# Kernel optimization log

Measured on AMD Instinct MI355X. Metric: run time of the kernel, lower is better.

Reference implementation:

```python
import jax, jax.numpy as jnp
import numpy as np

B, S, DM, DH, H, R = 2, 4096, 512, 512, 8, 4
HD = DH // H
SCALING = 1.0 / R  # alpha / r = 1.0 / 4


def setup_inputs() -> dict:
    key = jax.random.key(0)
    ks = jax.random.split(key, 12)
    lim = 1.0 / np.sqrt(DM)  # kaiming_uniform(a=sqrt(5)) bound for fan_in=DM
    inp = {
        "x": jax.random.normal(ks[0], (B, S, DM), dtype=jnp.float32),
        "atten_mask": jax.random.randint(ks[1], (B, S), 0, 2, dtype=jnp.int32),
        "Wk": jax.random.uniform(ks[2], (DH, DM), jnp.float32, -lim, lim),
        "Wq": jax.random.uniform(ks[3], (DH, DM), jnp.float32, -lim, lim),
        "Wv": jax.random.uniform(ks[4], (DH, DM), jnp.float32, -lim, lim),
        "Aq": jax.random.normal(ks[5], (R, DM), dtype=jnp.float32) * 0.01,
        "Bq": jax.random.normal(ks[6], (DH, R), dtype=jnp.float32) * 0.01,
        "Av": jax.random.normal(ks[7], (R, DM), dtype=jnp.float32) * 0.01,
        "Bv": jax.random.normal(ks[8], (DH, R), dtype=jnp.float32) * 0.01,
        "Wp": jax.random.uniform(ks[9], (DM, DH), jnp.float32, -1.0 / np.sqrt(DH), 1.0 / np.sqrt(DH)),
        "bp": jax.random.uniform(ks[10], (DM,), jnp.float32, -1.0 / np.sqrt(DH), 1.0 / np.sqrt(DH)),
    }
    return inp


def _heads(t):
    # [B,S,DH] -> [B,H,S,HD]
    return t.reshape(B, S, H, HD).transpose(0, 2, 1, 3)


def reference(x, atten_mask, Wk, Wq, Wv, Aq, Bq, Av, Bv, Wp, bp):
    k = x @ Wk.T
    q = x @ Wq.T + SCALING * ((x @ Aq.T) @ Bq.T)
    v = x @ Wv.T + SCALING * ((x @ Av.T) @ Bv.T)
    qh, kh, vh = _heads(q), _heads(k), _heads(v)
    scores = jnp.einsum("bhqd,bhkd->bhqk", qh, kh) / jnp.sqrt(jnp.float32(HD))
    neg = jnp.finfo(scores.dtype).min  # acts like -inf fill
    mask = (atten_mask == 0)[:, None, None, :]  # [B,1,1,S] over keys
    scores = jnp.where(mask, -jnp.inf, scores)
    probs = jax.nn.softmax(scores, axis=-1)
    ctx = jnp.einsum("bhqk,bhkd->bhqd", probs, vh)
    ctx = ctx.transpose(0, 2, 1, 3).reshape(B, S, DH)
    return ctx @ Wp.T + bp
```

## Files before the change

### kernel.cpp

```cpp
#include <hip/hip_runtime.h>
#include <hip/hip_bf16.h>
#include <stdint.h>

#define B_   2
#define S_   4096
#define DM_  512
#define DH_  512
#define H_   8
#define BS_  (B_*S_)
#define NX_  (BS_*DM_)
#define NW_  (DM_*DH_)
#define LOG2E 1.4426950408889634f
#define QSCALE (0.125f*LOG2E)

typedef __attribute__((ext_vector_type(4))) float f32x4;
typedef __attribute__((ext_vector_type(4))) short s16x4;
typedef __attribute__((ext_vector_type(8))) short s16x8;

__device__ __forceinline__ short f2bf(float x){
  uint32_t u = __builtin_bit_cast(uint32_t, x);
  u = (u + 0x7fffu + ((u >> 16) & 1u)) >> 16;
  return (short)u;
}
__device__ __forceinline__ float exp2fast(float x){ return __builtin_amdgcn_exp2f(x); }

__global__ __launch_bounds__(256) void convlora_kernel(
    const float* __restrict__ x,  const float* __restrict__ Wk,
    const float* __restrict__ Wq, const float* __restrict__ Wv,
    const float* __restrict__ Wp, const int* __restrict__ mask,
    const float* __restrict__ Aq, const float* __restrict__ Av,
    short* __restrict__ xbf,  short* __restrict__ wkbf, short* __restrict__ wqbf,
    short* __restrict__ wvbf, short* __restrict__ wpbf,
    float* __restrict__ biasw, float* __restrict__ Uq, float* __restrict__ Uv)
{
  const int bid = blockIdx.x;
  if (bid < 2560){
    const int tid = bid*256 + threadIdx.x;
    if (tid < BS_) biasw[tid] = mask[tid] ? 0.f : -1e30f;
    size_t idx = (size_t)tid*8;
    const float* src; short* dst; size_t off;
    if (idx < NX_)                      { src=x;  dst=xbf;  off=idx; }
    else if (idx < NX_+(size_t)NW_)     { src=Wk; dst=wkbf; off=idx-NX_; }
    else if (idx < NX_+2*(size_t)NW_)   { src=Wq; dst=wqbf; off=idx-NX_-NW_; }
    else if (idx < NX_+3*(size_t)NW_)   { src=Wv; dst=wvbf; off=idx-NX_-2*(size_t)NW_; }
    else                                { src=Wp; dst=wpbf; off=idx-NX_-3*(size_t)NW_; }
    f32x4 a = *(const f32x4*)(src+off);
    f32x4 b = *(const f32x4*)(src+off+4);
    s16x8 o;
    o[0]=f2bf(a.x); o[1]=f2bf(a.y); o[2]=f2bf(a.z); o[3]=f2bf(a.w);
    o[4]=f2bf(b.x); o[5]=f2bf(b.y); o[6]=f2bf(b.z); o[7]=f2bf(b.w);
    *(s16x8*)(dst+off) = o;
  } else {
    const int lane = threadIdx.x & 63, w = threadIdx.x >> 6;
    const int row = (bid-2560)*4 + w;
    const f32x4* xp = (const f32x4*)(x + (size_t)row*DM_ + lane*8);
    f32x4 x0 = xp[0], x1 = xp[1];
    float acc[8];
    #pragma unroll
    for (int r=0;r<4;r++){
      const f32x4* ap = (const f32x4*)(Aq + r*DM_ + lane*8);
      f32x4 a0 = ap[0], a1 = ap[1];
      const f32x4* vp = (const f32x4*)(Av + r*DM_ + lane*8);
      f32x4 b0 = vp[0], b1 = vp[1];
      acc[r]   = x0.x*a0.x + x0.y*a0.y + x0.z*a0.z + x0.w*a0.w
               + x1.x*a1.x + x1.y*a1.y + x1.z*a1.z + x1.w*a1.w;
      acc[4+r] = x0.x*b0.x + x0.y*b0.y + x0.z*b0.z + x0.w*b0.w
               + x1.x*b1.x + x1.y*b1.y + x1.z*b1.z + x1.w*b1.w;
    }
    #pragma unroll
    for (int i=0;i<8;i++){
      float v = acc[i];
      #pragma unroll
      for (int m=1;m<64;m<<=1) v += __shfl_xor(v, m);
      acc[i] = v;
    }
    if (lane == 0){
      #pragma unroll
      for (int r=0;r<4;r++){ Uq[row*4+r] = acc[r]; Uv[row*4+r] = acc[4+r]; }
    }
  }
}

__global__ __launch_bounds__(256) void qkv_kernel(
    const short* __restrict__ xbf,
    const short* __restrict__ wkbf, const short* __restrict__ wqbf,
    const short* __restrict__ wvbf,
    const float* __restrict__ Uq, const float* __restrict__ Bq,
    const float* __restrict__ Uv, const float* __restrict__ Bv,
    short* __restrict__ kw, short* __restrict__ qw, short* __restrict__ vw)
{
  __shared__ __align__(16) short As[128*32];
  __shared__ __align__(16) short Bsm[64*32];
  const int t = threadIdx.x;
  const int lane = t & 63, w = t >> 6;
  const int g = lane >> 4, l15 = lane & 15;
  const int m0 = blockIdx.x * 128;
  const int proj = blockIdx.y >> 3;
  const int n0 = (blockIdx.y & 7) * 64;
  const short* W = proj==0 ? wkbf : (proj==1 ? wqbf : wvbf);

  f32x4 acc[2][4];
  #pragma unroll
  for (int i=0;i<2;i++)
    #pragma unroll
    for (int j=0;j<4;j++){ f32x4 z = {0.f,0.f,0.f,0.f}; acc[i][j] = z; }

  const int rA0 = t >> 2,        sA0 = t & 3;
  const int rA1 = (t+256) >> 2,  sA1 = t & 3;
  const int rB  = t >> 2,        sB  = t & 3;

  const short* pa0 = xbf + (size_t)(m0+rA0)*DM_ + sA0*8;
  const short* pa1 = xbf + (size_t)(m0+rA1)*DM_ + sA1*8;
  const short* pbp = W   + (size_t)(n0+rB )*DM_ + sB *8;
  short* wa0 = (short*)((char*)As  + rA0*64 + ((sA0 ^ (rA0&3))*16));
  short* wa1 = (short*)((char*)As  + rA1*64 + ((sA1 ^ (rA1&3))*16));
  short* wb  = (short*)((char*)Bsm + rB *64 + ((sB  ^ (rB &3))*16));

  s16x8 va0 = *(const s16x8*)pa0; pa0 += 32;
  s16x8 va1 = *(const s16x8*)pa1; pa1 += 32;
  s16x8 vb  = *(const s16x8*)pbp; pbp += 32;

  for (int kt=0; kt<16; ++kt){
    __syncthreads();
    *(s16x8*)wa0 = va0;
    *(s16x8*)wa1 = va1;
    *(s16x8*)wb  = vb;
    __syncthreads();

    if (kt+1 < 16){
      va0 = *(const s16x8*)pa0; pa0 += 32;
      va1 = *(const s16x8*)pa1; pa1 += 32;
      vb  = *(const s16x8*)pbp; pbp += 32;
    }

    s16x8 af[2], bfr[4];
    #pragma unroll
    for (int mf=0; mf<2; ++mf){
      int rr = w*32 + mf*16 + l15;
      af[mf] = *(const s16x8*)((const char*)As + rr*64 + ((g ^ (rr&3))*16));
    }
    #pragma unroll
    for (int nf=0; nf<4; ++nf){
      int rr = nf*16 + l15;
      bfr[nf] = *(const s16x8*)((const char*)Bsm + rr*64 + ((g ^ (rr&3))*16));
    }
    __builtin_amdgcn_s_setprio(1);
    #pragma unroll
    for (int mf=0; mf<2; ++mf)
      #pragma unroll
      for (int nf=0; nf<4; ++nf)
        acc[mf][nf] = __builtin_amdgcn_mfma_f32_16x16x32_bf16(af[mf], bfr[nf], acc[mf][nf], 0, 0, 0);
    __builtin_amdgcn_s_setprio(0);
  }

  short* outp = proj==0 ? kw : (proj==1 ? qw : vw);
  const float* Um = (proj==1) ? Uq : Uv;
  const float* Bm = (proj==1) ? Bq : Bv;
  #pragma unroll
  for (int mf=0; mf<2; ++mf){
    #pragma unroll
    for (int r=0; r<4; ++r){
      const int m = m0 + w*32 + mf*16 + g*4 + r;
      f32x4 uvec = {0.f,0.f,0.f,0.f};
      if (proj) uvec = *(const f32x4*)(Um + m*4);
      #pragma unroll
      for (int nf=0; nf<4; ++nf){
        const int cn = n0 + nf*16 + l15;
        float val = acc[mf][nf][r];
        if (proj){
          f32x4 bb = *(const f32x4*)(Bm + cn*4);
          val += 0.25f*(uvec.x*bb.x + uvec.y*bb.y + uvec.z*bb.z + uvec.w*bb.w);
        }
        if (proj==1) val *= QSCALE;
        outp[(size_t)m*DH_ + cn] = f2bf(val);
      }
    }
  }
}

__global__ __launch_bounds__(256) void vt_kernel(const short* __restrict__ vw, short* __restrict__ vt){
  __shared__ __align__(16) short T[64*72];
  const int t = threadIdx.x;
  const int st = blockIdx.x, bh = blockIdx.y;
  const int b = bh >> 3, h = bh & 7;
  #pragma unroll
  for (int p=0;p<2;p++){
    int c = t + p*256;
    int row = c >> 3, off = c & 7;
    s16x8 v = *(const s16x8*)(vw + (size_t)(b*S_ + st*64 + row)*DH_ + h*64 + off*8);
    *(s16x8*)((char*)T + row*144 + off*16) = v;
  }
  __syncthreads();
  #pragma unroll
  for (int p=0;p<2;p++){
    int c = t + p*256;
    int d = c >> 3, soff = c & 7;
    s16x8 o;
    #pragma unroll
    for (int j=0;j<8;j++)
      o[j] = *((const short*)((const char*)T + (soff*8+j)*144 + d*2));
    *(s16x8*)(vt + (size_t)(bh*64 + d)*S_ + st*64 + soff*8) = o;
  }
}

__global__ __launch_bounds__(256) void attn_kernel(
    const short* __restrict__ qw, const short* __restrict__ kw,
    const short* __restrict__ vtw, const float* __restrict__ biasw,
    short* __restrict__ ctxw)
{
  __shared__ __align__(16) char smem[32768];
  short* Ks = (short*)smem;
  short* Vs = (short*)(smem + 8192);
  char*  Ps = smem + 16384;
  const int t = threadIdx.x, lane = t & 63, w = t >> 6;
  const int g = lane >> 4, l15 = lane & 15;
  const int bid = blockIdx.x;
  const int xcd = bid & 7, jj = bid >> 3;
  const int bh = xcd*2 + (jj >> 5), qb = jj & 31;
  const int b = bh >> 3, h = bh & 7;
  const int qr0 = qb*128 + w*32;

  s16x8 qf[2][2];
  #pragma unroll
  for (int tile=0;tile<2;tile++)
    #pragma unroll
    for (int ks=0;ks<2;ks++)
      qf[tile][ks] = *(const s16x8*)(qw + (size_t)(b*S_ + qr0 + tile*16 + l15)*DH_
                                     + h*64 + ks*32 + g*8);

  const float* gb = biasw + b*S_ + g*4;
  const short* kbase = kw + (size_t)(b*S_)*DH_ + h*64;
  const short* vbase = vtw + (size_t)(bh*64)*S_;
  char* Pw = Ps + w*4096;

  f32x4 ctx[2][5];
  #pragma unroll
  for (int tile=0;tile<2;tile++)
    #pragma unroll
    for (int n=0;n<5;n++){ f32x4 z = {0.f,0.f,0.f,0.f}; ctx[tile][n] = z; }

  const s16x8 ones = { 0x3F80,0x3F80,0x3F80,0x3F80,0x3F80,0x3F80,0x3F80,0x3F80 };

  const int c1 = t + 256;
  const int r0 = t >> 3,  o0 = t & 7;
  const int r1 = c1 >> 3, o1 = c1 & 7;
  const short* kp0 = kbase + (size_t)r0*DH_ + o0*8;
  const short* kp1 = kbase + (size_t)r1*DH_ + o1*8;
  const short* vp0 = vbase + (size_t)r0*S_ + o0*8;
  const short* vp1 = vbase + (size_t)r1*S_ + o1*8;
  char* wk0 = (char*)Ks + r0*128 + ((o0 ^ (r0&7))*16);
  char* wk1 = (char*)Ks + r1*128 + ((o1 ^ (r1&7))*16);
  char* wv0 = (char*)Vs + r0*128 + ((o0 ^ (r0&7))*16);
  char* wv1 = (char*)Vs + r1*128 + ((o1 ^ (r1&7))*16);

  s16x8 kv0 = *(const s16x8*)kp0; kp0 += 64*DH_;
  s16x8 kv1 = *(const s16x8*)kp1; kp1 += 64*DH_;
  s16x8 vv0 = *(const s16x8*)vp0; vp0 += 64;
  s16x8 vv1 = *(const s16x8*)vp1; vp1 += 64;
  f32x4 bvn[4];
  #pragma unroll
  for (int sb=0; sb<4; ++sb) bvn[sb] = *(const f32x4*)(gb + sb*16);

  for (int kt=0; kt<64; ++kt){
    __syncthreads();
    *(s16x8*)wk0 = kv0; *(s16x8*)wk1 = kv1;
    *(s16x8*)wv0 = vv0; *(s16x8*)wv1 = vv1;
    __syncthreads();

    f32x4 bv[4];
    #pragma unroll
    for (int sb=0; sb<4; ++sb) bv[sb] = bvn[sb];

    if (kt+1 < 64){
      kv0 = *(const s16x8*)kp0; kp0 += 64*DH_;
      kv1 = *(const s16x8*)kp1; kp1 += 64*DH_;
      vv0 = *(const s16x8*)vp0; vp0 += 64;
      vv1 = *(const s16x8*)vp1; vp1 += 64;
      const float* gn = gb + (kt+1)*64;
      #pragma unroll
      for (int sb=0; sb<4; ++sb) bvn[sb] = *(const f32x4*)(gn + sb*16);
    }

    f32x4 stA[4], stB[4];
    __builtin_amdgcn_s_setprio(1);
    #pragma unroll
    for (int sb=0; sb<4; ++sb){
      f32x4 sA = bv[sb], sB = bv[sb];
      #pragma unroll
      for (int ks=0; ks<2; ++ks){
        int row = sb*16 + l15;
        s16x8 kf = *(const s16x8*)((const char*)Ks + row*128 + (((ks*4+g) ^ (row&7))*16));
        sA = __builtin_amdgcn_mfma_f32_16x16x32_bf16(kf, qf[0][ks], sA, 0, 0, 0);
        sB = __builtin_amdgcn_mfma_f32_16x16x32_bf16(kf, qf[1][ks], sB, 0, 0, 0);
      }
      stA[sb] = sA; stB[sb] = sB;
    }
    __builtin_amdgcn_s_setprio(0);

    #pragma unroll
    for (int sb=0; sb<4; ++sb){
      int slot = (sb*2 + (g>>1)) ^ (l15 & 7);
      char* base = Pw + l15*128 + slot*16 + (g&1)*8;
      union { __hip_bfloat16 h[4]; s16x4 v; } cvA, cvB;
      cvA.h[0] = __float2bfloat16(exp2fast(stA[sb][0]));
      cvA.h[1] = __float2bfloat16(exp2fast(stA[sb][1]));
      cvA.h[2] = __float2bfloat16(exp2fast(stA[sb][2]));
      cvA.h[3] = __float2bfloat16(exp2fast(stA[sb][3]));
      cvB.h[0] = __float2bfloat16(exp2fast(stB[sb][0]));
      cvB.h[1] = __float2bfloat16(exp2fast(stB[sb][1]));
      cvB.h[2] = __float2bfloat16(exp2fast(stB[sb][2]));
      cvB.h[3] = __float2bfloat16(exp2fast(stB[sb][3]));
      *(s16x4*)(base)        = cvA.v;
      *(s16x4*)(base + 2048) = cvB.v;
    }

    __builtin_amdgcn_s_setprio(1);
    #pragma unroll
    for (int ks=0; ks<2; ++ks){
      const char* pb = Pw + l15*128 + (((ks*4+g) ^ (l15&7))*16);
      s16x8 pfA = *(const s16x8*)(pb);
      s16x8 pfB = *(const s16x8*)(pb + 2048);
      #pragma unroll
      for (int n=0;n<4;n++){
        int row = n*16 + l15;
        s16x8 vf = *(const s16x8*)((const char*)Vs + row*128 + (((ks*4+g) ^ (row&7))*16));
        ctx[0][n] = __builtin_amdgcn_mfma_f32_16x16x32_bf16(pfA, vf, ctx[0][n], 0, 0, 0);
        ctx[1][n] = __builtin_amdgcn_mfma_f32_16x16x32_bf16(pfB, vf, ctx[1][n], 0, 0, 0);
      }
      ctx[0][4] = __builtin_amdgcn_mfma_f32_16x16x32_bf16(pfA, ones, ctx[0][4], 0, 0, 0);
      ctx[1][4] = __builtin_amdgcn_mfma_f32_16x16x32_bf16(pfB, ones, ctx[1][4], 0, 0, 0);
    }
    __builtin_amdgcn_s_setprio(0);
  }

  #pragma unroll
  for (int tile=0;tile<2;tile++){
    float inv[4];
    #pragma unroll
    for (int r=0;r<4;r++) inv[r] = 1.f / ctx[tile][4][r];
    #pragma unroll
    for (int n=0;n<4;n++)
      #pragma unroll
      for (int r=0;r<4;r++){
        int m = b*S_ + qr0 + tile*16 + g*4 + r;
        ctxw[(size_t)m*DH_ + h*64 + n*16 + l15] = f2bf(ctx[tile][n][r] * inv[r]);
      }
  }
}

__global__ __launch_bounds__(256) void oproj_kernel(
    const short* __restrict__ ctxw, const short* __restrict__ wpbf,
    const float* __restrict__ bp, float* __restrict__ out)
{
  __shared__ __align__(16) short As[128*32];
  __shared__ __align__(16) short Bsm[64*32];
  const int t = threadIdx.x, lane = t & 63, w = t >> 6;
  const int g = lane >> 4, l15 = lane & 15;
  const int m0 = blockIdx.x*128, n0 = blockIdx.y*64;
  f32x4 acc[2][4];
  #pragma unroll
  for (int i=0;i<2;i++)
    #pragma unroll
    for (int j=0;j<4;j++){ f32x4 z = {0.f,0.f,0.f,0.f}; acc[i][j] = z; }

  const int rA0 = t >> 2,        sA0 = t & 3;
  const int rA1 = (t+256) >> 2,  sA1 = t & 3;
  const int rB  = t >> 2,        sB  = t & 3;

  const short* pa0 = ctxw + (size_t)(m0+rA0)*DH_ + sA0*8;
  const short* pa1 = ctxw + (size_t)(m0+rA1)*DH_ + sA1*8;
  const short* pbp = wpbf + (size_t)(n0+rB )*DH_ + sB *8;
  short* wa0 = (short*)((char*)As  + rA0*64 + ((sA0 ^ (rA0&3))*16));
  short* wa1 = (short*)((char*)As  + rA1*64 + ((sA1 ^ (rA1&3))*16));
  short* wb  = (short*)((char*)Bsm + rB *64 + ((sB  ^ (rB &3))*16));

  s16x8 va0 = *(const s16x8*)pa0; pa0 += 32;
  s16x8 va1 = *(const s16x8*)pa1; pa1 += 32;
  s16x8 vb  = *(const s16x8*)pbp; pbp += 32;

  for (int kt=0; kt<16; ++kt){
    __syncthreads();
    *(s16x8*)wa0 = va0;
    *(s16x8*)wa1 = va1;
    *(s16x8*)wb  = vb;
    __syncthreads();

    if (kt+1 < 16){
      va0 = *(const s16x8*)pa0; pa0 += 32;
      va1 = *(const s16x8*)pa1; pa1 += 32;
      vb  = *(const s16x8*)pbp; pbp += 32;
    }

    s16x8 af[2], bfr[4];
    #pragma unroll
    for (int mf=0; mf<2; ++mf){
      int rr = w*32 + mf*16 + l15;
      af[mf] = *(const s16x8*)((const char*)As + rr*64 + ((g ^ (rr&3))*16));
    }
    #pragma unroll
    for (int nf=0; nf<4; ++nf){
      int rr = nf*16 + l15;
      bfr[nf] = *(const s16x8*)((const char*)Bsm + rr*64 + ((g ^ (rr&3))*16));
    }
    __builtin_amdgcn_s_setprio(1);
    #pragma unroll
    for (int mf=0; mf<2; ++mf)
      #pragma unroll
      for (int nf=0; nf<4; ++nf)
        acc[mf][nf] = __builtin_amdgcn_mfma_f32_16x16x32_bf16(af[mf], bfr[nf], acc[mf][nf], 0, 0, 0);
    __builtin_amdgcn_s_setprio(0);
  }

  #pragma unroll
  for (int mf=0; mf<2; ++mf)
    #pragma unroll
    for (int nf=0; nf<4; ++nf){
      const int cn = n0 + nf*16 + l15;
      const float bpv = bp[cn];
      #pragma unroll
      for (int r=0;r<4;r++){
        const int m = m0 + w*32 + mf*16 + g*4 + r;
        out[(size_t)m*DM_ + cn] = acc[mf][nf][r] + bpv;
      }
    }
}

extern "C" void kernel_launch(void* const* d_in, const int* in_sizes, int n_in,
                              void* d_out, int out_size, void* d_ws, size_t ws_size,
                              hipStream_t stream)
{
  const float* x  = (const float*)d_in[0];
  const int* mask = (const int*)d_in[1];
  const float* Wk = (const float*)d_in[2];
  const float* Wq = (const float*)d_in[3];
  const float* Wv = (const float*)d_in[4];
  const float* Aq = (const float*)d_in[5];
  const float* Bq = (const float*)d_in[6];
  const float* Av = (const float*)d_in[7];
  const float* Bv = (const float*)d_in[8];
  const float* Wp = (const float*)d_in[9];
  const float* bp = (const float*)d_in[10];
  float* out = (float*)d_out;

  char* ws = (char*)d_ws;
  short* qw   = (short*)(ws);
  short* kw   = (short*)(ws + 8388608);
  short* vw   = (short*)(ws + 16777216);
  short* vtw  = (short*)(ws + 25165824);
  short* xbf  = (short*)(ws + 25165824);
  short* ctxw = (short*)(ws + 16777216);
  float* Uq   = (float*)(ws + 33554432);
  float* Uv   = (float*)(ws + 33685504);
  float* biasw= (float*)(ws + 33816576);
  short* wkbf = (short*)(ws + 33849344);
  short* wqbf = (short*)(ws + 34373632);
  short* wvbf = (short*)(ws + 34897920);
  short* wpbf = (short*)(ws + 35422208);

  convlora_kernel<<<dim3(4608), dim3(256), 0, stream>>>(
      x, Wk, Wq, Wv, Wp, mask, Aq, Av,
      xbf, wkbf, wqbf, wvbf, wpbf, biasw, Uq, Uv);
  qkv_kernel<<<dim3(64, 24), dim3(256), 0, stream>>>(xbf, wkbf, wqbf, wvbf,
                                                     Uq, Bq, Uv, Bv, kw, qw, vw);
  vt_kernel<<<dim3(64, 16), dim3(256), 0, stream>>>(vw, vtw);
  attn_kernel<<<dim3(512), dim3(256), 0, stream>>>(qw, kw, vtw, biasw, ctxw);
  oproj_kernel<<<dim3(64, 8), dim3(256), 0, stream>>>(ctxw, wpbf, bp, out);
  (void)in_sizes; (void)n_in; (void)out_size; (void)ws_size;
}
```

Measured before the change: 240.5 us.

## Split attention key range across two wave groups and merge partial results

```diff
diff --git a/kernel.cpp b/kernel.cpp
--- a/kernel.cpp
+++ b/kernel.cpp
@@ -203,22 +203,25 @@
   }
 }
 
-__global__ __launch_bounds__(256) void attn_kernel(
+__global__ __launch_bounds__(512) void attn_kernel(
     const short* __restrict__ qw, const short* __restrict__ kw,
     const short* __restrict__ vtw, const float* __restrict__ biasw,
     short* __restrict__ ctxw)
 {
-  __shared__ __align__(16) char smem[32768];
-  short* Ks = (short*)smem;
-  short* Vs = (short*)(smem + 8192);
-  char*  Ps = smem + 16384;
+  __shared__ __align__(16) char smem[65536];
   const int t = threadIdx.x, lane = t & 63, w = t >> 6;
   const int g = lane >> 4, l15 = lane & 15;
+  const int kvg = w >> 2, wq = w & 3;
   const int bid = blockIdx.x;
   const int xcd = bid & 7, jj = bid >> 3;
   const int bh = xcd*2 + (jj >> 5), qb = jj & 31;
   const int b = bh >> 3, h = bh & 7;
-  const int qr0 = qb*128 + w*32;
+  const int qr0 = qb*128 + wq*32;
+
+  short* Ks = (short*)(smem + kvg*16384);
+  short* Vs = (short*)(smem + kvg*16384 + 8192);
+  char*  Ps = smem + 32768;
+  char*  Pw = Ps + w*4096;
 
   s16x8 qf[2][2];
   #pragma unroll
@@ -228,10 +231,9 @@
       qf[tile][ks] = *(const s16x8*)(qw + (size_t)(b*S_ + qr0 + tile*16 + l15)*DH_
                                      + h*64 + ks*32 + g*8);
 
-  const float* gb = biasw + b*S_ + g*4;
-  const short* kbase = kw + (size_t)(b*S_)*DH_ + h*64;
-  const short* vbase = vtw + (size_t)(bh*64)*S_;
-  char* Pw = Ps + w*4096;
+  const float* gb = biasw + b*S_ + kvg*2048 + g*4;
+  const short* kbase = kw + (size_t)(b*S_ + kvg*2048)*DH_ + h*64;
+  const short* vbase = vtw + (size_t)(bh*64)*S_ + kvg*2048;
 
   f32x4 ctx[2][5];
   #pragma unroll
@@ -241,9 +243,10 @@
 
   const s16x8 ones = { 0x3F80,0x3F80,0x3F80,0x3F80,0x3F80,0x3F80,0x3F80,0x3F80 };
 
-  const int c1 = t + 256;
-  const int r0 = t >> 3,  o0 = t & 7;
-  const int r1 = c1 >> 3, o1 = c1 & 7;
+  const int tg = t & 255;
+  const int c1 = tg + 256;
+  const int r0 = tg >> 3,  o0 = tg & 7;
+  const int r1 = c1 >> 3,  o1 = c1 & 7;
   const short* kp0 = kbase + (size_t)r0*DH_ + o0*8;
   const short* kp1 = kbase + (size_t)r1*DH_ + o1*8;
   const short* vp0 = vbase + (size_t)r0*S_ + o0*8;
@@ -261,7 +264,7 @@
   #pragma unroll
   for (int sb=0; sb<4; ++sb) bvn[sb] = *(const f32x4*)(gb + sb*16);
 
-  for (int kt=0; kt<64; ++kt){
+  for (int kt=0; kt<32; ++kt){
     __syncthreads();
     *(s16x8*)wk0 = kv0; *(s16x8*)wk1 = kv1;
     *(s16x8*)wv0 = vv0; *(s16x8*)wv1 = vv1;
@@ -271,7 +274,7 @@
     #pragma unroll
     for (int sb=0; sb<4; ++sb) bv[sb] = bvn[sb];
 
-    if (kt+1 < 64){
+    if (kt+1 < 32){
       kv0 = *(const s16x8*)kp0; kp0 += 64*DH_;
       kv1 = *(const s16x8*)kp1; kp1 += 64*DH_;
       vv0 = *(const s16x8*)vp0; vp0 += 64;
@@ -333,18 +336,41 @@
     __builtin_amdgcn_s_setprio(0);
   }
 
-  #pragma unroll
-  for (int tile=0;tile<2;tile++){
-    float inv[4];
-    #pragma unroll
-    for (int r=0;r<4;r++) inv[r] = 1.f / ctx[tile][4][r];
-    #pragma unroll
-    for (int n=0;n<4;n++)
-      #pragma unroll
-      for (int r=0;r<4;r++){
-        int m = b*S_ + qr0 + tile*16 + g*4 + r;
-        ctxw[(size_t)m*DH_ + h*64 + n*16 + l15] = f2bf(ctx[tile][n][r] * inv[r]);
-      }
+  __syncthreads();
+  float* cbuf = (float*)smem;
+  const int cbase = (wq*64 + lane)*41;
+  if (kvg == 1){
+    #pragma unroll
+    for (int tile=0;tile<2;tile++)
+      #pragma unroll
+      for (int n=0;n<5;n++)
+        #pragma unroll
+        for (int r=0;r<4;r++)
+          cbuf[cbase + tile*20 + n*4 + r] = ctx[tile][n][r];
+  }
+  __syncthreads();
+  if (kvg == 0){
+    #pragma unroll
+    for (int tile=0;tile<2;tile++)
+      #pragma unroll
+      for (int n=0;n<5;n++)
+        #pragma unroll
+        for (int r=0;r<4;r++)
+          ctx[tile][n][r] += cbuf[cbase + tile*20 + n*4 + r];
+
+    #pragma unroll
+    for (int tile=0;tile<2;tile++){
+      float inv[4];
+      #pragma unroll
+      for (int r=0;r<4;r++) inv[r] = 1.f / ctx[tile][4][r];
+      #pragma unroll
+      for (int n=0;n<4;n++)
+        #pragma unroll
+        for (int r=0;r<4;r++){
+          int m = b*S_ + qr0 + tile*16 + g*4 + r;
+          ctxw[(size_t)m*DH_ + h*64 + n*16 + l15] = f2bf(ctx[tile][n][r] * inv[r]);
+        }
+    }
   }
 }
 
@@ -463,7 +489,7 @@
   qkv_kernel<<<dim3(64, 24), dim3(256), 0, stream>>>(xbf, wkbf, wqbf, wvbf,
                                                      Uq, Bq, Uv, Bv, kw, qw, vw);
   vt_kernel<<<dim3(64, 16), dim3(256), 0, stream>>>(vw, vtw);
-  attn_kernel<<<dim3(512), dim3(256), 0, stream>>>(qw, kw, vtw, biasw, ctxw);
+  attn_kernel<<<dim3(512), dim3(512), 0, stream>>>(qw, kw, vtw, biasw, ctxw);
   oproj_kernel<<<dim3(64, 8), dim3(256), 0, stream>>>(ctxw, wpbf, bp, out);
   (void)in_sizes; (void)n_in; (void)out_size; (void)ws_size;
 }
```

After: 232.9 us. 1.03x faster.
